# Kernel optimization log

Hardware: AMD Instinct MI355X
Metric: run time of the kernel (lower is better)

## Reference

```python
import jax, jax.numpy as jnp
import numpy as np

N_SONGS = 100000   # vocab size; also the padding id
EMBED = 64
B = 1024
L = 200


def setup_inputs() -> dict:
    key = jax.random.key(0)
    k1, k2, k3, k4 = jax.random.split(key, 4)
    songs = jax.random.randint(k1, (B, L), 0, N_SONGS)            # valid ids in [0, N_SONGS)
    lengths = jax.random.randint(k2, (B,), 1, L + 1)              # ragged per-sample lengths
    pos = jnp.arange(L)
    songs = jnp.where(pos[None, :] < lengths[:, None], songs, N_SONGS)  # pad tail with N_SONGS
    emb_table = jax.random.normal(k3, (N_SONGS, EMBED), dtype=jnp.float32) * 0.02
    W = jax.random.normal(k4, (N_SONGS, EMBED), dtype=jnp.float32) * 0.02
    b = jnp.zeros((N_SONGS,), dtype=jnp.float32)
    return {"songs": songs, "emb_table": emb_table, "W": W, "b": b}


def reference(songs, emb_table, W, b):
    # Vectorized equivalent of the per-sample Python loop:
    # mask out padding id (== N_SONGS), gather embeddings, mean over valid,
    # Linear(embed_dim -> n_songs) + sigmoid.
    mask = songs != N_SONGS                               # [B, L] bool
    safe_ids = jnp.where(mask, songs, 0)                  # clamp pads to a valid index
    emb = emb_table[safe_ids] * mask[..., None].astype(emb_table.dtype)  # [B, L, D]
    count = jnp.sum(mask, axis=1, keepdims=True).astype(emb_table.dtype)  # [B, 1]
    pooled = jnp.sum(emb, axis=1) / count                 # [B, D] masked mean
    logits = pooled @ W.T + b                             # [B, N_SONGS]
    return jax.nn.sigmoid(logits)
```

## Files before the change

kernel.cpp:

```cpp
#include <hip/hip_runtime.h>
#include <hip/hip_bf16.h>
#include <cstdint>
#include <cstddef>

#define N_SONGS 100000
#define EMBED   64
#define BATCH   1024
#define SEQL    200

typedef __attribute__((ext_vector_type(8)))  __bf16 bf16x8;
typedef __attribute__((ext_vector_type(16))) float  f32x16;
typedef __attribute__((ext_vector_type(4)))  float  f32x4;

__device__ __forceinline__ unsigned short f2b_rne(float x) {
    union { float f; uint32_t u; } v; v.f = x;
    uint32_t u = v.u;
    return (unsigned short)((u + 0x7FFFu + ((u >> 16) & 1u)) >> 16);
}

__global__ __launch_bounds__(256) void prep_kernel(const float* __restrict__ W,
                                                   unsigned short* __restrict__ wbf,
                                                   const int* __restrict__ songs,
                                                   const float* __restrict__ emb,
                                                   unsigned short* __restrict__ pooled) {
    __shared__ float part[4][EMBED];
    __shared__ int   cnts[4];

    if (blockIdx.x < 2048) {
        const int n4 = (N_SONGS * EMBED) / 4;
        int i = blockIdx.x * 256 + threadIdx.x;
        for (; i < n4; i += 2048 * 256) {
            f32x4 v = __builtin_nontemporal_load(&((const f32x4*)W)[i]);
            ushort4 o;
            o.x = f2b_rne(v.x); o.y = f2b_rne(v.y);
            o.z = f2b_rne(v.z); o.w = f2b_rne(v.w);
            ((ushort4*)wbf)[i] = o;
        }
    } else {
        int b = blockIdx.x - 2048;
        int t = threadIdx.x;
        int d = t & 63;
        int c = t >> 6;

        const int* row = songs + (size_t)b * SEQL;
        float acc = 0.f;
        int cnt = 0;
        int l0 = c * (SEQL / 4);
        for (int l = l0; l < l0 + SEQL / 4; ++l) {
            int id = row[l];
            if (id != N_SONGS) {
                acc += emb[(size_t)id * EMBED + d];
                ++cnt;
            }
        }
        part[c][d] = acc;
        if (d == 0) cnts[c] = cnt;
        __syncthreads();
        if (t < EMBED) {
            float s = part[0][t] + part[1][t] + part[2][t] + part[3][t];
            float n = (float)(cnts[0] + cnts[1] + cnts[2] + cnts[3]);
            pooled[(size_t)b * EMBED + t] = f2b_rne(s / n);
        }
    }
}

__global__ __launch_bounds__(256, 2) void gemm_kernel(const unsigned short* __restrict__ pooled,
                                                      const unsigned short* __restrict__ wbf,
                                                      const float* __restrict__ bias,
                                                      float* __restrict__ out) {
    int nt = blockIdx.x, mt = blockIdx.y;
    int t = threadIdx.x;
    int w = t >> 6, lane = t & 63;
    int wm = w >> 1, wn = w & 1;
    int lc = lane & 31;
    int hi = lane >> 5;

    int m0 = mt * 128 + wm * 64;
    int n0 = nt * 128 + wn * 64;

    bf16x8 afrag[4][2];
#pragma unroll
    for (int ks = 0; ks < 4; ++ks)
#pragma unroll
        for (int mi = 0; mi < 2; ++mi) {
            const unsigned short* p =
                pooled + (size_t)(m0 + mi * 32 + lc) * EMBED + ks * 16 + hi * 8;
            afrag[ks][mi] = *(const bf16x8*)p;
        }

    bf16x8 bfrag[4][2];
#pragma unroll
    for (int ks = 0; ks < 4; ++ks)
#pragma unroll
        for (int nj = 0; nj < 2; ++nj) {
            int n = n0 + nj * 32 + lc;
            n = n < N_SONGS ? n : N_SONGS - 1;
            const unsigned short* p = wbf + (size_t)n * EMBED + ks * 16 + hi * 8;
            bfrag[ks][nj] = *(const bf16x8*)p;
        }

    f32x16 acc[2][2];
#pragma unroll
    for (int mi = 0; mi < 2; ++mi)
#pragma unroll
        for (int nj = 0; nj < 2; ++nj)
#pragma unroll
            for (int r = 0; r < 16; ++r)
                acc[mi][nj][r] = 0.f;

#pragma unroll
    for (int ks = 0; ks < 4; ++ks)
#pragma unroll
        for (int mi = 0; mi < 2; ++mi)
#pragma unroll
            for (int nj = 0; nj < 2; ++nj)
                acc[mi][nj] = __builtin_amdgcn_mfma_f32_32x32x16_bf16(
                    afrag[ks][mi], bfrag[ks][nj], acc[mi][nj], 0, 0, 0);

#pragma unroll
    for (int nj = 0; nj < 2; ++nj) {
        int n = n0 + nj * 32 + lc;
        if (n >= N_SONGS) continue;
        float bv = bias[n];
#pragma unroll
        for (int mi = 0; mi < 2; ++mi) {
#pragma unroll
            for (int r = 0; r < 16; ++r) {
                int row = m0 + mi * 32 + (r & 3) + 8 * (r >> 2) + 4 * hi;
                float x = acc[mi][nj][r] + bv;
                float e = __expf(-x);
                float s = __builtin_amdgcn_rcpf(1.0f + e);
                __builtin_nontemporal_store(s, &out[(size_t)row * N_SONGS + n]);
            }
        }
    }
}

extern "C" void kernel_launch(void* const* d_in, const int* in_sizes, int n_in,
                              void* d_out, int out_size, void* d_ws, size_t ws_size,
                              hipStream_t stream) {
    const int*   songs = (const int*)d_in[0];
    const float* emb   = (const float*)d_in[1];
    const float* W     = (const float*)d_in[2];
    const float* bias  = (const float*)d_in[3];
    float* out = (float*)d_out;

    unsigned short* wbf    = (unsigned short*)d_ws;
    unsigned short* pooled = wbf + (size_t)N_SONGS * EMBED;

    hipLaunchKernelGGL(prep_kernel, dim3(2048 + BATCH), dim3(256), 0, stream,
                       W, wbf, songs, emb, pooled);
    hipLaunchKernelGGL(gemm_kernel,
                       dim3((N_SONGS + 127) / 128, BATCH / 128), dim3(256), 0, stream,
                       pooled, wbf, bias, out);
}
```

Measured before the change: 112.5 us.

## Fuse W bf16 conversion into GEMM loads and remap tiles for L2 reuse

Removes the separate pass that converted the full fp32 W matrix to bf16 in workspace; the GEMM now loads fp32 W rows directly and converts them to bf16 in registers. The prep kernel shrinks to just the pooling work. The GEMM grid becomes 1D with a block-index remap that spreads the 8 M-tiles of one N-tile across block indices. This removes a full write and re-read of W, at the cost of doubled W read bytes per tile, repeated by the 8 M-tile blocks, which rely on L2 hits.

```diff
diff --git a/kernel.cpp b/kernel.cpp
--- a/kernel.cpp
+++ b/kernel.cpp
@@ -7,6 +7,8 @@
 #define EMBED   64
 #define BATCH   1024
 #define SEQL    200
+#define NTILES  782
+#define GBLOCKS (NTILES * 8)
 
 typedef __attribute__((ext_vector_type(8)))  __bf16 bf16x8;
 typedef __attribute__((ext_vector_type(16))) float  f32x16;
@@ -18,57 +20,45 @@
     return (unsigned short)((u + 0x7FFFu + ((u >> 16) & 1u)) >> 16);
 }
 
-__global__ __launch_bounds__(256) void prep_kernel(const float* __restrict__ W,
-                                                   unsigned short* __restrict__ wbf,
-                                                   const int* __restrict__ songs,
+__global__ __launch_bounds__(256) void pool_kernel(const int* __restrict__ songs,
                                                    const float* __restrict__ emb,
                                                    unsigned short* __restrict__ pooled) {
     __shared__ float part[4][EMBED];
     __shared__ int   cnts[4];
 
-    if (blockIdx.x < 2048) {
-        const int n4 = (N_SONGS * EMBED) / 4;
-        int i = blockIdx.x * 256 + threadIdx.x;
-        for (; i < n4; i += 2048 * 256) {
-            f32x4 v = __builtin_nontemporal_load(&((const f32x4*)W)[i]);
-            ushort4 o;
-            o.x = f2b_rne(v.x); o.y = f2b_rne(v.y);
-            o.z = f2b_rne(v.z); o.w = f2b_rne(v.w);
-            ((ushort4*)wbf)[i] = o;
+    int b = blockIdx.x;
+    int t = threadIdx.x;
+    int d = t & 63;
+    int c = t >> 6;
+
+    const int* row = songs + (size_t)b * SEQL;
+    float acc = 0.f;
+    int cnt = 0;
+    int l0 = c * (SEQL / 4);
+    for (int l = l0; l < l0 + SEQL / 4; ++l) {
+        int id = row[l];
+        if (id != N_SONGS) {
+            acc += emb[(size_t)id * EMBED + d];
+            ++cnt;
         }
-    } else {
-        int b = blockIdx.x - 2048;
-        int t = threadIdx.x;
-        int d = t & 63;
-        int c = t >> 6;
-
-        const int* row = songs + (size_t)b * SEQL;
-        float acc = 0.f;
-        int cnt = 0;
-        int l0 = c * (SEQL / 4);
-        for (int l = l0; l < l0 + SEQL / 4; ++l) {
-            int id = row[l];
-            if (id != N_SONGS) {
-                acc += emb[(size_t)id * EMBED + d];
-                ++cnt;
-            }
-        }
-        part[c][d] = acc;
-        if (d == 0) cnts[c] = cnt;
-        __syncthreads();
-        if (t < EMBED) {
-            float s = part[0][t] + part[1][t] + part[2][t] + part[3][t];
-            float n = (float)(cnts[0] + cnts[1] + cnts[2] + cnts[3]);
-            pooled[(size_t)b * EMBED + t] = f2b_rne(s / n);
-        }
+    }
+    part[c][d] = acc;
+    if (d == 0) cnts[c] = cnt;
+    __syncthreads();
+    if (t < EMBED) {
+        float s = part[0][t] + part[1][t] + part[2][t] + part[3][t];
+        float n = (float)(cnts[0] + cnts[1] + cnts[2] + cnts[3]);
+        pooled[(size_t)b * EMBED + t] = f2b_rne(s / n);
     }
 }
 
 __global__ __launch_bounds__(256, 2) void gemm_kernel(const unsigned short* __restrict__ pooled,
-                                                      const unsigned short* __restrict__ wbf,
+                                                      const float* __restrict__ W,
                                                       const float* __restrict__ bias,
                                                       float* __restrict__ out) {
-    int nt = blockIdx.x, mt = blockIdx.y;
+    int idx = (blockIdx.x & 7) * NTILES + (blockIdx.x >> 3);
+    int nt = idx >> 3, mt = idx & 7;
+
     int t = threadIdx.x;
     int w = t >> 6, lane = t & 63;
     int wm = w >> 1, wn = w & 1;
@@ -95,8 +85,13 @@
         for (int nj = 0; nj < 2; ++nj) {
             int n = n0 + nj * 32 + lc;
             n = n < N_SONGS ? n : N_SONGS - 1;
-            const unsigned short* p = wbf + (size_t)n * EMBED + ks * 16 + hi * 8;
-            bfrag[ks][nj] = *(const bf16x8*)p;
+            const float* p = W + (size_t)n * EMBED + ks * 16 + hi * 8;
+            f32x4 v0 = *(const f32x4*)p;
+            f32x4 v1 = *(const f32x4*)(p + 4);
+            bf16x8 r;
+#pragma unroll
+            for (int e = 0; e < 4; ++e) { r[e] = (__bf16)v0[e]; r[e + 4] = (__bf16)v1[e]; }
+            bfrag[ks][nj] = r;
         }
 
     f32x16 acc[2][2];
@@ -145,12 +140,10 @@
     const float* bias  = (const float*)d_in[3];
     float* out = (float*)d_out;
 
-    unsigned short* wbf    = (unsigned short*)d_ws;
-    unsigned short* pooled = wbf + (size_t)N_SONGS * EMBED;
+    unsigned short* pooled = (unsigned short*)d_ws;
 
-    hipLaunchKernelGGL(prep_kernel, dim3(2048 + BATCH), dim3(256), 0, stream,
-                       W, wbf, songs, emb, pooled);
-    hipLaunchKernelGGL(gemm_kernel,
-                       dim3((N_SONGS + 127) / 128, BATCH / 128), dim3(256), 0, stream,
-                       pooled, wbf, bias, out);
+    hipLaunchKernelGGL(pool_kernel, dim3(BATCH), dim3(256), 0, stream,
+                       songs, emb, pooled);
+    hipLaunchKernelGGL(gemm_kernel, dim3(GBLOCKS), dim3(256), 0, stream,
+                       pooled, W, bias, out);
 }
```

New measurement: 123.2 us. 1.09x slower.

## Stage GEMM output tile in LDS for coalesced 16-byte row stores

Applied to the files above, without the earlier changes.

Reshapes the GEMM tile from 128x128 to 32 rows by 512 columns, with each wave covering 128 columns. The sigmoid results are written to a 64KB shared-memory tile, then stored with float4 nontemporal writes along contiguous output rows. This targets the scattered 4-byte strided stores of the old epilogue on the dominant 400MB output write. In exchange it adds a barrier, LDS traffic and 64KB of LDS per block, which may lower occupancy. It also reloads W fragments once per 32-row M tile instead of once per 128 rows.

```diff
diff --git a/kernel.cpp b/kernel.cpp
--- a/kernel.cpp
+++ b/kernel.cpp
@@ -68,70 +68,75 @@
                                                       const unsigned short* __restrict__ wbf,
                                                       const float* __restrict__ bias,
                                                       float* __restrict__ out) {
+    __shared__ float tile[32 * 512];
+
     int nt = blockIdx.x, mt = blockIdx.y;
     int t = threadIdx.x;
     int w = t >> 6, lane = t & 63;
-    int wm = w >> 1, wn = w & 1;
     int lc = lane & 31;
     int hi = lane >> 5;
 
-    int m0 = mt * 128 + wm * 64;
-    int n0 = nt * 128 + wn * 64;
+    int m0 = mt * 32;
+    int n0 = nt * 512;
+    int nw = n0 + w * 128;
 
-    bf16x8 afrag[4][2];
+    bf16x8 afrag[4];
+#pragma unroll
+    for (int ks = 0; ks < 4; ++ks) {
+        const unsigned short* p =
+            pooled + (size_t)(m0 + lc) * EMBED + ks * 16 + hi * 8;
+        afrag[ks] = *(const bf16x8*)p;
+    }
+
+    bf16x8 bfrag[4][4];
 #pragma unroll
     for (int ks = 0; ks < 4; ++ks)
 #pragma unroll
-        for (int mi = 0; mi < 2; ++mi) {
-            const unsigned short* p =
-                pooled + (size_t)(m0 + mi * 32 + lc) * EMBED + ks * 16 + hi * 8;
-            afrag[ks][mi] = *(const bf16x8*)p;
-        }
-
-    bf16x8 bfrag[4][2];
-#pragma unroll
-    for (int ks = 0; ks < 4; ++ks)
-#pragma unroll
-        for (int nj = 0; nj < 2; ++nj) {
-            int n = n0 + nj * 32 + lc;
+        for (int nj = 0; nj < 4; ++nj) {
+            int n = nw + nj * 32 + lc;
             n = n < N_SONGS ? n : N_SONGS - 1;
             const unsigned short* p = wbf + (size_t)n * EMBED + ks * 16 + hi * 8;
             bfrag[ks][nj] = *(const bf16x8*)p;
         }
 
-    f32x16 acc[2][2];
+    f32x16 acc[4];
 #pragma unroll
-    for (int mi = 0; mi < 2; ++mi)
+    for (int nj = 0; nj < 4; ++nj)
 #pragma unroll
-        for (int nj = 0; nj < 2; ++nj)
-#pragma unroll
-            for (int r = 0; r < 16; ++r)
-                acc[mi][nj][r] = 0.f;
+        for (int r = 0; r < 16; ++r)
+            acc[nj][r] = 0.f;
 
 #pragma unroll
     for (int ks = 0; ks < 4; ++ks)
 #pragma unroll
-        for (int mi = 0; mi < 2; ++mi)
-#pragma unroll
-            for (int nj = 0; nj < 2; ++nj)
-                acc[mi][nj] = __builtin_amdgcn_mfma_f32_32x32x16_bf16(
-                    afrag[ks][mi], bfrag[ks][nj], acc[mi][nj], 0, 0, 0);
+        for (int nj = 0; nj < 4; ++nj)
+            acc[nj] = __builtin_amdgcn_mfma_f32_32x32x16_bf16(
+                afrag[ks], bfrag[ks][nj], acc[nj], 0, 0, 0);
 
 #pragma unroll
-    for (int nj = 0; nj < 2; ++nj) {
-        int n = n0 + nj * 32 + lc;
-        if (n >= N_SONGS) continue;
-        float bv = bias[n];
+    for (int nj = 0; nj < 4; ++nj) {
+        int ncol = nw + nj * 32 + lc;
+        float bv = bias[ncol < N_SONGS ? ncol : N_SONGS - 1];
+        int col = w * 128 + nj * 32 + lc;
 #pragma unroll
-        for (int mi = 0; mi < 2; ++mi) {
+        for (int r = 0; r < 16; ++r) {
+            int row = (r & 3) + 8 * (r >> 2) + 4 * hi;
+            float x = acc[nj][r] + bv;
+            float e = __expf(-x);
+            tile[row * 512 + col] = __builtin_amdgcn_rcpf(1.0f + e);
+        }
+    }
+    __syncthreads();
+
 #pragma unroll
-            for (int r = 0; r < 16; ++r) {
-                int row = m0 + mi * 32 + (r & 3) + 8 * (r >> 2) + 4 * hi;
-                float x = acc[mi][nj][r] + bv;
-                float e = __expf(-x);
-                float s = __builtin_amdgcn_rcpf(1.0f + e);
-                __builtin_nontemporal_store(s, &out[(size_t)row * N_SONGS + n]);
-            }
+    for (int i = 0; i < 16; ++i) {
+        int c = i * 256 + t;
+        int row = c >> 7;
+        int cir = c & 127;
+        int col = n0 + cir * 4;
+        if (col < N_SONGS) {
+            f32x4 v = *(const f32x4*)&tile[c * 4];
+            __builtin_nontemporal_store(v, (f32x4*)&out[(size_t)(m0 + row) * N_SONGS + col]);
         }
     }
 }
@@ -151,6 +156,6 @@
     hipLaunchKernelGGL(prep_kernel, dim3(2048 + BATCH), dim3(256), 0, stream,
                        W, wbf, songs, emb, pooled);
     hipLaunchKernelGGL(gemm_kernel,
-                       dim3((N_SONGS + 127) / 128, BATCH / 128), dim3(256), 0, stream,
+                       dim3((N_SONGS + 511) / 512, BATCH / 32), dim3(256), 0, stream,
                        pooled, wbf, bias, out);
 }
```

After: 137.8 us. 1.22x slower.
